# Optimization experiments

Hardware: AMD Instinct MI355X
Metric: run time of the kernel (lower is better)

The kernel has to match this reference:

```python
import jax, jax.numpy as jnp
import numpy as np

B, L, D, NH, V, T, CYC = 16, 512, 512, 8, 8000, 17, 2
HD = D // NH


def _attn(q, kv, qw, qb, kw, kb, vw, vb, ow, ob):
    # q: [N, Lq, D], kv: [N, Lk, D]; weights stored [in, out] (= torch W.T)
    N, Lq, _ = q.shape
    Lk = kv.shape[1]
    Q = (q @ qw + qb).reshape(N, Lq, NH, HD)
    K = (kv @ kw + kb).reshape(N, Lk, NH, HD)
    Vv = (kv @ vw + vb).reshape(N, Lk, NH, HD)
    scores = jnp.einsum('nqhd,nkhd->nhqk', Q, K) / np.float32(np.sqrt(HD))
    probs = jax.nn.softmax(scores, axis=-1)
    ctx = jnp.einsum('nhqk,nkhd->nqhd', probs, Vv).reshape(N, Lq, D)
    return ctx @ ow + ob


def _ln(x, w, b, eps=1e-12):
    u = x.mean(-1, keepdims=True)
    s = ((x - u) ** 2).mean(-1, keepdims=True)
    return w * (x - u) / jnp.sqrt(s + eps) + b


def setup_inputs() -> dict:
    key = jax.random.key(0)
    ks = jax.random.split(key, 32)
    p = {}
    p['tokens'] = jax.random.randint(ks[0], (B, L, 1), 0, V)
    p['masks'] = jnp.ones((B, L), dtype=jnp.int64)
    p['heads'] = jax.random.randint(ks[1], (B, L), 0, 2)
    p['tails'] = jax.random.randint(ks[2], (B, L), 0, 2)
    p['char_emb'] = jax.random.normal(ks[3], (V, D), jnp.float32) * 0.02
    i = 4
    for pre in ('sat', 'rel'):
        for nm in ('q', 'k', 'v', 'o'):
            p[f'{pre}_{nm}w'] = jax.random.normal(ks[i], (D, D), jnp.float32) * 0.02
            p[f'{pre}_{nm}b'] = jnp.zeros((D,), jnp.float32)
            i += 1
    p['ln_sat_w'] = jnp.ones((D,), jnp.float32)
    p['ln_sat_b'] = jnp.zeros((D,), jnp.float32)
    p['ln_rel_w'] = jnp.ones((D,), jnp.float32)
    p['ln_rel_b'] = jnp.zeros((D,), jnp.float32)
    p['ofc_w'] = jax.random.normal(ks[i], (D, T), jnp.float32) * 0.02
    p['ofc_b'] = jnp.zeros((T,), jnp.float32)
    return p


def reference(tokens, masks, heads, tails, char_emb,
              sat_qw, sat_qb, sat_kw, sat_kb, sat_vw, sat_vb, sat_ow, sat_ob,
              rel_qw, rel_qb, rel_kw, rel_kb, rel_vw, rel_vb, rel_ow, rel_ob,
              ln_sat_w, ln_sat_b, ln_rel_w, ln_rel_b, ofc_w, ofc_b):
    e = char_emb[tokens[:, :, 0]]  # [B, L, D]
    h = e
    s = e.mean(axis=1)  # relay token [B, D] (avg_pool2d over seq)
    for _ in range(CYC):
        # backward cycle_shift in the source is a correct roll-by-(-1)
        h_last = jnp.roll(h, -1, axis=1)
        # forward cycle_shift in the source is sequential in-place: result[:,0]=h[:,-1],
        # result[:,i>=1]=h[:,0] (the write at i=0 propagates). Reproduced faithfully.
        h_next = jnp.concatenate(
            [h[:, -1:, :], jnp.broadcast_to(h[:, :1, :], (B, L - 1, D))], axis=1)
        sm = jnp.broadcast_to(s[:, None, :], (B, L, D))
        c = jnp.stack([h_last, h, h_next, e, sm], axis=2).reshape(B * L, 5, D)
        hq = h.reshape(B * L, 1, D)
        a = _attn(hq, c, sat_qw, sat_qb, sat_kw, sat_kb, sat_vw, sat_vb, sat_ow, sat_ob)
        h = _ln(jax.nn.relu(a), ln_sat_w, ln_sat_b).reshape(B, L, D)
        mc = jnp.concatenate([s[:, None, :], h], axis=1)  # [B, L+1, D]
        r = _attn(s[:, None, :], mc, rel_qw, rel_qb, rel_kw, rel_kb, rel_vw, rel_vb, rel_ow, rel_ob)
        s = _ln(jax.nn.relu(r), ln_rel_w, ln_rel_b)[:, 0, :]
    logits = h @ ofc_w + ofc_b  # [B, L, T]
    return logits
```

## Files before the change

kernel.cpp:

```cpp
#include <hip/hip_runtime.h>
#include <hip/hip_bf16.h>

typedef __hip_bfloat16 bf16;

#define BB 16
#define LL 512
#define DD 512
#define NHH 8
#define HDD 64
#define TT 17
#define MM (BB*LL)
#define RCH 8
#define RCK 65

typedef __attribute__((ext_vector_type(8))) short bfrag;
typedef __attribute__((ext_vector_type(4))) float ffrag;
typedef __attribute__((ext_vector_type(8))) unsigned short us8;

static __device__ __forceinline__ void gld16(const void* g, void* l){
  __builtin_amdgcn_global_load_lds((const __attribute__((address_space(1))) void*)g,
                                   (__attribute__((address_space(3))) void*)l, 16, 0, 0);
}
static __device__ __forceinline__ float us2f(unsigned short u){
  unsigned int v = ((unsigned int)u) << 16;
  float f; __builtin_memcpy(&f, &v, 4); return f;
}
static __device__ __forceinline__ float hsum8(float v){
  v += __shfl_xor(v, 1);
  v += __shfl_xor(v, 2);
  v += __shfl_xor(v, 4);
  return v;
}

__global__ __launch_bounds__(256)
void emean(const int* __restrict__ tokens, const float* __restrict__ emb,
           bf16* __restrict__ ebf, float* __restrict__ mpart){
  int blk = blockIdx.x;
  int b = blk >> 4, lc = blk & 15;
  int t = threadIdx.x;
  __shared__ int toks[32];
  if (t < 32) toks[t] = tokens[b*LL + lc*32 + t];
  __syncthreads();
  bf16* eb = ebf + ((size_t)b*LL + lc*32)*DD;
  for (int d = t; d < DD; d += 256){
    float acc = 0.f;
    #pragma unroll 4
    for (int l = 0; l < 32; l++){
      float v = emb[(size_t)toks[l]*DD + d];
      eb[(size_t)l*DD + d] = __float2bfloat16(v);
      acc += v;
    }
    mpart[(size_t)blk*DD + d] = acc;
  }
}
__global__ void mean2(const float* __restrict__ part, float* __restrict__ s){
  int i = blockIdx.x*256 + threadIdx.x;
  int b = i >> 9, d = i & 511;
  float acc = 0.f;
  #pragma unroll
  for (int c = 0; c < 16; c++) acc += part[(size_t)(b*16 + c)*DD + d];
  s[i] = acc * (1.0f/LL);
}

__global__ void prep_w(const float* __restrict__ i0, const float* __restrict__ i1,
                       const float* __restrict__ i2, const float* __restrict__ i3,
                       const float* __restrict__ i4, const float* __restrict__ i5,
                       const float* __restrict__ wlog,
                       bf16* __restrict__ o0, bf16* __restrict__ o1,
                       bf16* __restrict__ o2, bf16* __restrict__ o3,
                       bf16* __restrict__ o4, bf16* __restrict__ o5,
                       bf16* __restrict__ olog){
  int z = blockIdx.z;
  int tx = threadIdx.x, ty = threadIdx.y;
  if (z == 6){
    int tid = ty*32 + tx;
    int i = ((blockIdx.y*16 + blockIdx.x) << 8) + tid;
    int row = i >> 9, k = i & 511;
    olog[i] = __float2bfloat16(row < TT ? wlog[(size_t)k*TT + row] : 0.f);
    return;
  }
  __shared__ float tile[32][33];
  const float* in = (z==0)?i0:(z==1)?i1:(z==2)?i2:(z==3)?i3:(z==4)?i4:i5;
  bf16* out       = (z==0)?o0:(z==1)?o1:(z==2)?o2:(z==3)?o3:(z==4)?o4:o5;
  int bx = blockIdx.x*32, by = blockIdx.y*32;
  #pragma unroll
  for (int j = 0; j < 32; j += 8)
    tile[ty + j][tx] = in[(size_t)(by + ty + j)*DD + bx + tx];
  __syncthreads();
  #pragma unroll
  for (int j = 0; j < 32; j += 8)
    out[(size_t)(bx + ty + j)*DD + by + tx] = __float2bfloat16(tile[tx][ty + j]);
}

__global__ __launch_bounds__(256)
void gemm_mfma_bf(const bf16* __restrict__ A, const bf16* __restrict__ Wt,
                  const float* __restrict__ b0, const float* __restrict__ b1,
                  const float* __restrict__ b2, const float* __restrict__ b3,
                  const float* __restrict__ b4,
                  bf16* __restrict__ D0, int ld0,
                  bf16* __restrict__ D1, int ld1, int split){
  const int K = 512;
  __shared__ bf16 As[128*32];
  __shared__ bf16 Bs[128*32];
  int t = threadIdx.x;
  int wave = t >> 6, lane = t & 63;
  int id = blockIdx.x;
  int bm = (((id & 7) << 3) | ((id >> 3) & 7)) * 128;
  int bn = (id >> 6) * 128;
  int wm = (wave & 1) * 64, wn = (wave >> 1) * 64;
  ffrag acc[4][4];
  #pragma unroll
  for (int i = 0; i < 4; i++)
    #pragma unroll
    for (int j = 0; j < 4; j++) acc[i][j] = (ffrag){0.f,0.f,0.f,0.f};

  int srow = t >> 2;
  int scol = (t & 3) * 8;
  const bf16* gA = A  + (size_t)(bm + srow)*K + scol;
  const bf16* gB = Wt + (size_t)(bn + srow)*K + scol;
  char* lA = (char*)As + 16*t;
  char* lB = (char*)Bs + 16*t;
  int q = lane >> 4, r = lane & 15;

  for (int k0 = 0; k0 < K; k0 += 32){
    gld16(gA + k0,          lA);
    gld16(gA + 64*K + k0,   lA + 4096);
    gld16(gB + k0,          lB);
    gld16(gB + 64*K + k0,   lB + 4096);
    __syncthreads();
    bfrag af[4], bfv[4];
    #pragma unroll
    for (int i = 0; i < 4; i++){
      af[i]  = *(const bfrag*)(As + (wm + i*16 + r)*32 + q*8);
      bfv[i] = *(const bfrag*)(Bs + (wn + i*16 + r)*32 + q*8);
    }
    #pragma unroll
    for (int i = 0; i < 4; i++)
      #pragma unroll
      for (int j = 0; j < 4; j++)
        acc[i][j] = __builtin_amdgcn_mfma_f32_16x16x32_bf16(af[i], bfv[j], acc[i][j], 0, 0, 0);
    __syncthreads();
  }
  #pragma unroll
  for (int i = 0; i < 4; i++){
    #pragma unroll
    for (int j = 0; j < 4; j++){
      int row = bm + wm + i*16 + q*4;
      int col = bn + wn + j*16 + r;
      const float* bp = (col < 512) ? b0 : (col < 1024) ? b1 :
                        (col < 1536) ? b2 : (col < 2048) ? b3 : b4;
      float bias = bp[col & 511];
      bf16* D; int ld;
      if (col < split){ D = D0 + (size_t)row*ld0 + col;         ld = ld0; }
      else            { D = D1 + (size_t)row*ld1 + (col-split); ld = ld1; }
      #pragma unroll
      for (int g = 0; g < 4; g++)
        D[(size_t)g*ld] = __float2bfloat16(acc[i][j][g] + bias);
    }
  }
}

__global__ __launch_bounds__(256)
void gemm_logits(const bf16* __restrict__ A, const bf16* __restrict__ Wt,
                 const float* __restrict__ bias, float* __restrict__ C){
  const int K = 512;
  __shared__ bf16 As[128*32];
  __shared__ bf16 Bs[128*32];
  int t = threadIdx.x;
  int wave = t >> 6, lane = t & 63;
  int bm = blockIdx.y * 128;
  int wm = (wave & 1) * 64, wn = (wave >> 1) * 64;
  ffrag acc[2];
  acc[0] = (ffrag){0.f,0.f,0.f,0.f};
  acc[1] = (ffrag){0.f,0.f,0.f,0.f};

  int srow = t >> 2;
  int scol = (t & 3) * 8;
  const bf16* gA = A  + (size_t)(bm + srow)*K + scol;
  const bf16* gB = Wt + (size_t)srow*K + scol;
  char* lA = (char*)As + 16*t;
  char* lB = (char*)Bs + 16*t;
  int q = lane >> 4, r = lane & 15;

  for (int k0 = 0; k0 < K; k0 += 32){
    gld16(gA + k0,          lA);
    gld16(gA + 64*K + k0,   lA + 4096);
    gld16(gB + k0,          lB);
    gld16(gB + 64*K + k0,   lB + 4096);
    __syncthreads();
    if (wn == 0){
      #pragma unroll
      for (int i = 0; i < 4; i++){
        bfrag af = *(const bfrag*)(As + (wm + i*16 + r)*32 + q*8);
        if (i < 2){
          bfrag bfv = *(const bfrag*)(Bs + (i*16 + r)*32 + q*8);
        }
      }
      bfrag bf0 = *(const bfrag*)(Bs + (0*16 + r)*32 + q*8);
      bfrag bf1 = *(const bfrag*)(Bs + (1*16 + r)*32 + q*8);
      #pragma unroll
      for (int i = 0; i < 4; i++){
        bfrag af = *(const bfrag*)(As + (wm + i*16 + r)*32 + q*8);
        (void)af; (void)bf0; (void)bf1;
      }
    }
    __syncthreads();
  }
  (void)acc; (void)bias; (void)C; (void)wn;
}

__global__ __launch_bounds__(256)
void gemm_logits2(const bf16* __restrict__ A, const bf16* __restrict__ Wt,
                  const float* __restrict__ bias, float* __restrict__ C){
  const int K = 512;
  __shared__ bf16 As[128*32];
  __shared__ bf16 Bs[128*32];
  int t = threadIdx.x;
  int wave = t >> 6, lane = t & 63;
  int bm = blockIdx.y * 128;
  int wm = (wave & 1) * 64, wn = (wave >> 1) * 64;
  ffrag acc[4][2];
  #pragma unroll
  for (int i = 0; i < 4; i++){ acc[i][0] = (ffrag){0,0,0,0}; acc[i][1] = (ffrag){0,0,0,0}; }

  int srow = t >> 2;
  int scol = (t & 3) * 8;
  const bf16* gA = A  + (size_t)(bm + srow)*K + scol;
  const bf16* gB = Wt + (size_t)srow*K + scol;
  char* lA = (char*)As + 16*t;
  char* lB = (char*)Bs + 16*t;
  int q = lane >> 4, r = lane & 15;

  for (int k0 = 0; k0 < K; k0 += 32){
    gld16(gA + k0,          lA);
    gld16(gA + 64*K + k0,   lA + 4096);
    gld16(gB + k0,          lB);
    gld16(gB + 64*K + k0,   lB + 4096);
    __syncthreads();
    if (wn == 0){
      bfrag bf0 = *(const bfrag*)(Bs + (r)*32 + q*8);
      bfrag bf1 = *(const bfrag*)(Bs + (16 + r)*32 + q*8);
      #pragma unroll
      for (int i = 0; i < 4; i++){
        bfrag af = *(const bfrag*)(As + (wm + i*16 + r)*32 + q*8);
        acc[i][0] = __builtin_amdgcn_mfma_f32_16x16x32_bf16(af, bf0, acc[i][0], 0, 0, 0);
        acc[i][1] = __builtin_amdgcn_mfma_f32_16x16x32_bf16(af, bf1, acc[i][1], 0, 0, 0);
      }
    }
    __syncthreads();
  }
  if (wn == 0){
    #pragma unroll
    for (int i = 0; i < 4; i++){
      #pragma unroll
      for (int j = 0; j < 2; j++){
        int row = bm + wm + i*16 + q*4;
        int col = j*16 + r;
        if (col < TT){
          float bias_v = bias[col];
          #pragma unroll
          for (int g = 0; g < 4; g++)
            C[(size_t)(row + g)*TT + col] = acc[i][j][g] + bias_v;
        }
      }
    }
  }
}

__global__ __launch_bounds__(256)
void s_proj(const float* __restrict__ A,
            const float* __restrict__ W0, const float* __restrict__ W1,
            const float* __restrict__ W2, const float* __restrict__ W3,
            const float* __restrict__ W4,
            const float* __restrict__ bias0, const float* __restrict__ bias1,
            const float* __restrict__ bias2, const float* __restrict__ bias3,
            const float* __restrict__ bias4,
            float* __restrict__ O0, float* __restrict__ O1,
            float* __restrict__ O2, float* __restrict__ O3,
            float* __restrict__ O4,
            int ldc0, int ldc1, int ldc2, int ldc3, int ldc4){
  __shared__ float part[8][32][17];
  int t = threadIdx.x;
  int n = t & 31, kg = t >> 5;
  int wi = blockIdx.x >> 4, ch = blockIdx.x & 15;
  const float* W  = (wi==0)?W0:(wi==1)?W1:(wi==2)?W2:(wi==3)?W3:W4;
  const float* bs = (wi==0)?bias0:(wi==1)?bias1:(wi==2)?bias2:(wi==3)?bias3:bias4;
  float* O  = (wi==0)?O0:(wi==1)?O1:(wi==2)?O2:(wi==3)?O3:O4;
  int ldc   = (wi==0)?ldc0:(wi==1)?ldc1:(wi==2)?ldc2:(wi==3)?ldc3:ldc4;
  int col = ch*32 + n;
  float acc[16];
  #pragma unroll
  for (int m = 0; m < 16; m++) acc[m] = 0.f;
  const float* Wp = W + (size_t)(kg*64)*512 + col;
  const float* Ap = A + kg*64;
  for (int k = 0; k < 64; k++){
    float w = Wp[(size_t)k*512];
    #pragma unroll
    for (int m = 0; m < 16; m++) acc[m] = fmaf(Ap[m*512 + k], w, acc[m]);
  }
  #pragma unroll
  for (int m = 0; m < 16; m++) part[kg][n][m] = acc[m];
  __syncthreads();
  for (int o = t; o < 512; o += 256){
    int m = o >> 5, nn = o & 31;
    float v = 0.f;
    #pragma unroll
    for (int g = 0; g < 8; g++) v += part[g][nn][m];
    O[(size_t)m*ldc + ch*32 + nn] = v + bs[ch*32 + nn];
  }
}

__global__ __launch_bounds__(256)
void sat_attn(const bf16* __restrict__ qp, int sq,
              const bf16* __restrict__ kp, const bf16* __restrict__ vp, int skv,
              const bf16* __restrict__ KeVe, const float* __restrict__ KsVs,
              bf16* __restrict__ ctx){
  int tok = blockIdx.x*4 + (threadIdx.x >> 6);
  int l = threadIdx.x & 63;
  int b = tok >> 9, li = tok & 511;
  int off = l*8;
  int t0 = (b << 9) | ((li + 1) & 511);
  int t2 = (b << 9) | (li == 0 ? 511 : 0);

  float qf[8];
  { us8 q8 = *(const us8*)(qp + (size_t)tok*sq + off);
    #pragma unroll
    for (int g = 0; g < 8; g++) qf[g] = us2f(q8[g]); }

  float sc[5];
  int rows[3] = {t0, tok, t2};
  #pragma unroll
  for (int j = 0; j < 3; j++){
    us8 k8 = *(const us8*)(kp + (size_t)rows[j]*skv + off);
    float a = 0.f;
    #pragma unroll
    for (int g = 0; g < 8; g++) a += qf[g]*us2f(k8[g]);
    sc[j] = hsum8(a) * 0.125f;
  }
  { us8 k8 = *(const us8*)(KeVe + (size_t)tok*1024 + off);
    float a = 0.f;
    #pragma unroll
    for (int g = 0; g < 8; g++) a += qf[g]*us2f(k8[g]);
    sc[3] = hsum8(a) * 0.125f; }
  { const float* ks = KsVs + (size_t)b*1024 + off;
    float4 f0 = *(const float4*)ks, f1 = *(const float4*)(ks + 4);
    float a = qf[0]*f0.x + qf[1]*f0.y + qf[2]*f0.z + qf[3]*f0.w
            + qf[4]*f1.x + qf[5]*f1.y + qf[6]*f1.z + qf[7]*f1.w;
    sc[4] = hsum8(a) * 0.125f; }

  float m = fmaxf(fmaxf(fmaxf(sc[0],sc[1]), fmaxf(sc[2],sc[3])), sc[4]);
  float p[5], den = 0.f;
  #pragma unroll
  for (int j = 0; j < 5; j++){ p[j] = __expf(sc[j]-m); den += p[j]; }
  float inv = 1.0f/den;

  float o[8];
  #pragma unroll
  for (int g = 0; g < 8; g++) o[g] = 0.f;
  #pragma unroll
  for (int j = 0; j < 3; j++){
    us8 v8 = *(const us8*)(vp + (size_t)rows[j]*skv + off);
    #pragma unroll
    for (int g = 0; g < 8; g++) o[g] += p[j]*us2f(v8[g]);
  }
  { us8 v8 = *(const us8*)(KeVe + (size_t)tok*1024 + 512 + off);
    #pragma unroll
    for (int g = 0; g < 8; g++) o[g] += p[3]*us2f(v8[g]); }
  { const float* vs = KsVs + (size_t)b*1024 + 512 + off;
    float4 f0 = *(const float4*)vs, f1 = *(const float4*)(vs + 4);
    o[0] += p[4]*f0.x; o[1] += p[4]*f0.y; o[2] += p[4]*f0.z; o[3] += p[4]*f0.w;
    o[4] += p[4]*f1.x; o[5] += p[4]*f1.y; o[6] += p[4]*f1.z; o[7] += p[4]*f1.w; }

  bf16 ob[8];
  #pragma unroll
  for (int g = 0; g < 8; g++) ob[g] = __float2bfloat16(o[g]*inv);
  *(us8*)(ctx + (size_t)tok*DD + off) = *(const us8*)ob;
}

__global__ __launch_bounds__(256)
void rel_part(const float* __restrict__ q, const float* __restrict__ Ksr,
              const float* __restrict__ Vsr, const bf16* __restrict__ KV,
              float* __restrict__ pws){
  int ch = blockIdx.x, hh = blockIdx.y, b = blockIdx.z;
  int t = threadIdx.x;
  int base = hh * HDD;
  __shared__ __align__(16) float qs[64];
  __shared__ float sc[RCK];
  __shared__ float red[256];
  __shared__ float part[4][64];
  int j0 = ch * RCK;
  int nk = min(513 - j0, RCK);
  if (t < 64) qs[t] = q[(size_t)b*DD + base + t];
  __syncthreads();
  if (t < nk){
    int j = j0 + t;
    float a = 0.f;
    if (j == 0){
      const float* kr = Ksr + (size_t)b*DD + base;
      #pragma unroll
      for (int d = 0; d < 64; d += 4){
        float4 k4 = *(const float4*)(kr + d);
        float4 q4 = *(const float4*)(qs + d);
        a += q4.x*k4.x + q4.y*k4.y + q4.z*k4.z + q4.w*k4.w;
      }
    } else {
      const bf16* kr = KV + ((size_t)b*LL + j - 1)*1024 + base;
      #pragma unroll
      for (int d = 0; d < 64; d += 8){
        us8 k8 = *(const us8*)(kr + d);
        #pragma unroll
        for (int g = 0; g < 8; g++) a += qs[d+g] * us2f(k8[g]);
      }
    }
    sc[t] = a * 0.125f;
  }
  __syncthreads();
  red[t] = (t < nk) ? sc[t] : -1e30f; __syncthreads();
  for (int st = 128; st; st >>= 1){ if (t < st) red[t] = fmaxf(red[t], red[t+st]); __syncthreads(); }
  float m = red[0]; __syncthreads();
  if (t < nk) sc[t] = __expf(sc[t] - m);
  __syncthreads();
  red[t] = (t < nk) ? sc[t] : 0.f; __syncthreads();
  for (int st = 128; st; st >>= 1){ if (t < st) red[t] += red[t+st]; __syncthreads(); }
  float l = red[0];
  int d = t & 63, c2 = t >> 6;
  float a = 0.f;
  for (int j = c2; j < nk; j += 4){
    int gj = j0 + j;
    float vv = (gj == 0) ? Vsr[(size_t)b*DD + base + d]
                         : __bfloat162float(KV[((size_t)b*LL + gj - 1)*1024 + 512 + base + d]);
    a += sc[j] * vv;
  }
  part[c2][d] = a; __syncthreads();
  float* o = pws + (((size_t)(b*NHH + hh))*RCH + ch) * 66;
  if (t < 64) o[t] = part[0][t] + part[1][t] + part[2][t] + part[3][t];
  else if (t == 64) o[64] = m;
  else if (t == 65) o[65] = l;
}

__global__ __launch_bounds__(256)
void rel_tail(const float* __restrict__ pws, const float* __restrict__ W,
              const float* __restrict__ bias, const float* __restrict__ lnw,
              const float* __restrict__ lnb, float* __restrict__ s){
  int b = blockIdx.x;
  int t = threadIdx.x;
  __shared__ float crs[512];
  __shared__ float red[256];
  for (int o = t; o < 512; o += 256){
    int hh = o >> 6, d = o & 63;
    const float* p = pws + ((size_t)(b*NHH + hh))*RCH*66;
    float M = -1e30f;
    #pragma unroll
    for (int c = 0; c < RCH; c++) M = fmaxf(M, p[c*66 + 64]);
    float den = 0.f, acc = 0.f;
    #pragma unroll
    for (int c = 0; c < RCH; c++){
      float w = __expf(p[c*66 + 64] - M);
      den += w * p[c*66 + 65];
      acc += w * p[c*66 + d];
    }
    crs[o] = acc / den;
  }
  __syncthreads();
  int n0 = t, n1 = t + 256;
  float a0 = 0.f, a1 = 0.f;
  for (int k = 0; k < 512; k++){
    float c = crs[k];
    a0 = fmaf(c, W[(size_t)k*512 + n0], a0);
    a1 = fmaf(c, W[(size_t)k*512 + n1], a1);
  }
  a0 += bias[n0]; a1 += bias[n1];
  float v0 = fmaxf(a0, 0.f), v1 = fmaxf(a1, 0.f);
  red[t] = v0 + v1; __syncthreads();
  for (int st = 128; st; st >>= 1){ if (t < st) red[t] += red[t+st]; __syncthreads(); }
  float u = red[0] * (1.0f/DD); __syncthreads();
  float d0 = v0 - u, d1 = v1 - u;
  red[t] = d0*d0 + d1*d1; __syncthreads();
  for (int st = 128; st; st >>= 1){ if (t < st) red[t] += red[t+st]; __syncthreads(); }
  float inv = rsqrtf(red[0] * (1.0f/DD) + 1e-12f);
  s[(size_t)b*DD + n0] = lnw[n0]*d0*inv + lnb[n0];
  s[(size_t)b*DD + n1] = lnw[n1]*d1*inv + lnb[n1];
}

__global__ void relu_ln_bf(const bf16* __restrict__ X, const float* __restrict__ w,
                           const float* __restrict__ bn, bf16* __restrict__ Ybf){
  int row = blockIdx.x;
  int tid = threadIdx.x;
  __shared__ float red[256];
  const bf16* x = X + (size_t)row*DD;
  float v0 = fmaxf(__bfloat162float(x[tid]), 0.f);
  float v1 = fmaxf(__bfloat162float(x[tid+256]), 0.f);
  red[tid] = v0 + v1;
  __syncthreads();
  for (int st = 128; st; st >>= 1){ if (tid < st) red[tid] += red[tid+st]; __syncthreads(); }
  float u = red[0] * (1.0f/DD);
  __syncthreads();
  float d0 = v0 - u, d1 = v1 - u;
  red[tid] = d0*d0 + d1*d1;
  __syncthreads();
  for (int st = 128; st; st >>= 1){ if (tid < st) red[tid] += red[tid+st]; __syncthreads(); }
  float var = red[0] * (1.0f/DD);
  float inv = rsqrtf(var + 1e-12f);
  Ybf[(size_t)row*DD + tid]       = __float2bfloat16(w[tid]    *d0*inv + bn[tid]);
  Ybf[(size_t)row*DD + tid + 256] = __float2bfloat16(w[tid+256]*d1*inv + bn[tid+256]);
}

extern "C" void kernel_launch(void* const* d_in, const int* in_sizes, int n_in,
                              void* d_out, int out_size, void* d_ws, size_t ws_size,
                              hipStream_t stream) {
  const int*   tokens  = (const int*)  d_in[0];
  const float* emb     = (const float*)d_in[4];
  const float* sat_qw  = (const float*)d_in[5];
  const float* sat_qb  = (const float*)d_in[6];
  const float* sat_kw  = (const float*)d_in[7];
  const float* sat_kb  = (const float*)d_in[8];
  const float* sat_vw  = (const float*)d_in[9];
  const float* sat_vb  = (const float*)d_in[10];
  const float* sat_ow  = (const float*)d_in[11];
  const float* sat_ob  = (const float*)d_in[12];
  const float* rel_qw  = (const float*)d_in[13];
  const float* rel_qb  = (const float*)d_in[14];
  const float* rel_kw  = (const float*)d_in[15];
  const float* rel_kb  = (const float*)d_in[16];
  const float* rel_vw  = (const float*)d_in[17];
  const float* rel_vb  = (const float*)d_in[18];
  const float* rel_ow  = (const float*)d_in[19];
  const float* rel_ob  = (const float*)d_in[20];
  const float* ln_sat_w= (const float*)d_in[21];
  const float* ln_sat_b= (const float*)d_in[22];
  const float* ln_rel_w= (const float*)d_in[23];
  const float* ln_rel_b= (const float*)d_in[24];
  const float* ofc_w   = (const float*)d_in[25];
  const float* ofc_b   = (const float*)d_in[26];

  char* p = (char*)d_ws;
  auto alloc = [&](size_t bytes) -> char* {
    char* r = p; p += (bytes + 255) & ~(size_t)255; return r;
  };
  const size_t BIGH = (size_t)MM*DD*2;
  bf16*  ebf   = (bf16*) alloc(BIGH);
  bf16*  qkv   = (bf16*) alloc(3*BIGH);
  bf16*  kvbuf = (bf16*) alloc(2*BIGH);
  bf16*  KeVe  = (bf16*) alloc(2*BIGH);
  bf16*  qbuf  = (bf16*) alloc(BIGH);
  bf16*  ctxbf = (bf16*) alloc(BIGH);
  bf16*  WtAll = (bf16*) alloc((size_t)2560*512*2);
  bf16*  WtO   = (bf16*) alloc((size_t)512*512*2);
  bf16*  WtLog = (bf16*) alloc((size_t)128*512*2);
  float* s     = (float*)alloc(BB*DD*4);
  float* KsVs  = (float*)alloc(BB*1024*4);
  float* qr    = (float*)alloc(BB*DD*4);
  float* Ksr   = (float*)alloc(BB*DD*4);
  float* Vsr   = (float*)alloc(BB*DD*4);
  float* mpart = (float*)alloc((size_t)256*DD*4);
  float* pws   = (float*)alloc((size_t)BB*NHH*RCH*66*4);
  bf16*  hbf   = ebf;
  bf16*  aout  = qkv;

  emean<<<256, 256, 0, stream>>>(tokens, emb, ebf, mpart);
  mean2<<<32, 256, 0, stream>>>(mpart, s);

  prep_w<<<dim3(16,16,7), dim3(32,8), 0, stream>>>(
      sat_qw, sat_kw, sat_vw, rel_kw, rel_vw, sat_ow, ofc_w,
      WtAll, WtAll + (size_t)512*512, WtAll + (size_t)1024*512,
      WtAll + (size_t)1536*512, WtAll + (size_t)2048*512, WtO, WtLog);

  gemm_mfma_bf<<<12*64, 256, 0, stream>>>(ebf, WtAll,
      sat_qb, sat_kb, sat_vb, sat_vb, sat_vb, qbuf, 512, KeVe, 1024, 512);
  s_proj<<<80, 256, 0, stream>>>(s,
      sat_kw, sat_vw, rel_qw, rel_kw, rel_vw,
      sat_kb, sat_vb, rel_qb, rel_kb, rel_vb,
      KsVs, KsVs + 512, qr, Ksr, Vsr,
      1024, 1024, 512, 512, 512);
  sat_attn<<<MM/4, 256, 0, stream>>>(qbuf, 512, KeVe, KeVe + 512, 1024,
                                     KeVe, KsVs, ctxbf);
  gemm_mfma_bf<<<4*64, 256, 0, stream>>>(ctxbf, WtO,
      sat_ob, sat_ob, sat_ob, sat_ob, sat_ob, aout, 512, aout, 512, 512);
  relu_ln_bf<<<MM, 256, 0, stream>>>(aout, ln_sat_w, ln_sat_b, hbf);
  gemm_mfma_bf<<<20*64, 256, 0, stream>>>(hbf, WtAll,
      sat_qb, sat_kb, sat_vb, rel_kb, rel_vb, qkv, 1536, kvbuf, 1024, 1536);
  rel_part<<<dim3(RCH, NHH, BB), 256, 0, stream>>>(qr, Ksr, Vsr, kvbuf, pws);
  rel_tail<<<BB, 256, 0, stream>>>(pws, rel_ow, rel_ob, ln_rel_w, ln_rel_b, s);

  s_proj<<<32, 256, 0, stream>>>(s,
      sat_kw, sat_vw, sat_vw, sat_vw, sat_vw,
      sat_kb, sat_vb, sat_vb, sat_vb, sat_vb,
      KsVs, KsVs + 512, Ksr, Ksr, Ksr,
      1024, 1024, 512, 512, 512);
  sat_attn<<<MM/4, 256, 0, stream>>>(qkv, 1536, qkv + 512, qkv + 1024, 1536,
                                     KeVe, KsVs, ctxbf);
  gemm_mfma_bf<<<4*64, 256, 0, stream>>>(ctxbf, WtO,
      sat_ob, sat_ob, sat_ob, sat_ob, sat_ob, aout, 512, aout, 512, 512);
  relu_ln_bf<<<MM, 256, 0, stream>>>(aout, ln_sat_w, ln_sat_b, hbf);

  gemm_logits2<<<dim3(1,64), 256, 0, stream>>>(hbf, WtLog, ofc_b, (float*)d_out);
}
```

Before: 336.3 us.

## Fuse whole forward into one cooperative persistent megakernel with grid syncs

Replaces the sequence of separate kernel launches with a single cooperative kernel that runs each stage as work units over a persistent grid, separated by grid-wide barriers. A per-launch fallback path is kept. It also swizzles the LDS column layout in the GEMM tiles to reduce bank conflicts. The s-projection is restructured so each batch row is handled by one block with a serial K loop. The aim is to remove launch gaps between stages, at the cost of grid-sync overhead, a grid capped at about two blocks per CU for large stages, and a slower single-block fp32 s-projection.

```diff
diff --git a/kernel.cpp b/kernel.cpp
--- a/kernel.cpp
+++ b/kernel.cpp
@@ -1,6 +1,8 @@
 #include <hip/hip_runtime.h>
 #include <hip/hip_bf16.h>
-
+#include <hip/hip_cooperative_groups.h>
+
+namespace cg = cooperative_groups;
 typedef __hip_bfloat16 bf16;
 
 #define BB 16
@@ -17,6 +19,16 @@
 typedef __attribute__((ext_vector_type(4))) float ffrag;
 typedef __attribute__((ext_vector_type(8))) unsigned short us8;
 
+struct Params {
+  const int* tokens;
+  const float* emb;
+  const float *sat_qw, *sat_qb, *sat_kw, *sat_kb, *sat_vw, *sat_vb, *sat_ow, *sat_ob;
+  const float *rel_qw, *rel_qb, *rel_kw, *rel_kb, *rel_vw, *rel_vb, *rel_ow, *rel_ob;
+  const float *ln_sat_w, *ln_sat_b, *ln_rel_w, *ln_rel_b, *ofc_w, *ofc_b;
+  bf16 *ebf, *qkv, *kvbuf, *KeVe, *qbuf, *ctxbf, *WtAll, *WtO, *WtLog;
+  float *KsVs, *qr, *Ksr, *Vsr, *mpart, *pws, *out;
+};
+
 static __device__ __forceinline__ void gld16(const void* g, void* l){
   __builtin_amdgcn_global_load_lds((const __attribute__((address_space(1))) void*)g,
                                    (__attribute__((address_space(3))) void*)l, 16, 0, 0);
@@ -26,63 +38,43 @@
   float f; __builtin_memcpy(&f, &v, 4); return f;
 }
 static __device__ __forceinline__ float hsum8(float v){
-  v += __shfl_xor(v, 1);
-  v += __shfl_xor(v, 2);
-  v += __shfl_xor(v, 4);
+  v += __shfl_xor(v, 1); v += __shfl_xor(v, 2); v += __shfl_xor(v, 4);
   return v;
 }
 
-__global__ __launch_bounds__(256)
-void emean(const int* __restrict__ tokens, const float* __restrict__ emb,
-           bf16* __restrict__ ebf, float* __restrict__ mpart){
-  int blk = blockIdx.x;
-  int b = blk >> 4, lc = blk & 15;
-  int t = threadIdx.x;
-  __shared__ int toks[32];
-  if (t < 32) toks[t] = tokens[b*LL + lc*32 + t];
-  __syncthreads();
-  bf16* eb = ebf + ((size_t)b*LL + lc*32)*DD;
+static __device__ void emean_unit(int u, int t, char* sm, const Params& P){
+  int* toks = (int*)sm;
+  int b = u >> 4, lc = u & 15;
+  if (t < 32) toks[t] = P.tokens[b*LL + lc*32 + t];
+  __syncthreads();
+  bf16* eb = P.ebf + ((size_t)b*LL + lc*32)*DD;
   for (int d = t; d < DD; d += 256){
     float acc = 0.f;
     #pragma unroll 4
     for (int l = 0; l < 32; l++){
-      float v = emb[(size_t)toks[l]*DD + d];
+      float v = P.emb[(size_t)toks[l]*DD + d];
       eb[(size_t)l*DD + d] = __float2bfloat16(v);
       acc += v;
     }
-    mpart[(size_t)blk*DD + d] = acc;
-  }
-}
-__global__ void mean2(const float* __restrict__ part, float* __restrict__ s){
-  int i = blockIdx.x*256 + threadIdx.x;
-  int b = i >> 9, d = i & 511;
-  float acc = 0.f;
-  #pragma unroll
-  for (int c = 0; c < 16; c++) acc += part[(size_t)(b*16 + c)*DD + d];
-  s[i] = acc * (1.0f/LL);
-}
-
-__global__ void prep_w(const float* __restrict__ i0, const float* __restrict__ i1,
-                       const float* __restrict__ i2, const float* __restrict__ i3,
-                       const float* __restrict__ i4, const float* __restrict__ i5,
-                       const float* __restrict__ wlog,
-                       bf16* __restrict__ o0, bf16* __restrict__ o1,
-                       bf16* __restrict__ o2, bf16* __restrict__ o3,
-                       bf16* __restrict__ o4, bf16* __restrict__ o5,
-                       bf16* __restrict__ olog){
-  int z = blockIdx.z;
-  int tx = threadIdx.x, ty = threadIdx.y;
+    P.mpart[(size_t)u*DD + d] = acc;
+  }
+  __syncthreads();
+}
+
+static __device__ void prep_unit(int u, int t, char* sm, const Params& P){
+  int z = u >> 8, xy = u & 255;
+  int tx = t & 31, ty = t >> 5;
   if (z == 6){
-    int tid = ty*32 + tx;
-    int i = ((blockIdx.y*16 + blockIdx.x) << 8) + tid;
+    int i = (xy << 8) + t;
     int row = i >> 9, k = i & 511;
-    olog[i] = __float2bfloat16(row < TT ? wlog[(size_t)k*TT + row] : 0.f);
+    P.WtLog[i] = __float2bfloat16(row < TT ? P.ofc_w[(size_t)k*TT + row] : 0.f);
     return;
   }
-  __shared__ float tile[32][33];
-  const float* in = (z==0)?i0:(z==1)?i1:(z==2)?i2:(z==3)?i3:(z==4)?i4:i5;
-  bf16* out       = (z==0)?o0:(z==1)?o1:(z==2)?o2:(z==3)?o3:(z==4)?o4:o5;
-  int bx = blockIdx.x*32, by = blockIdx.y*32;
+  float (*tile)[33] = (float(*)[33])sm;
+  const float* in = (z==0)?P.sat_qw:(z==1)?P.sat_kw:(z==2)?P.sat_vw:
+                    (z==3)?P.rel_kw:(z==4)?P.rel_vw:P.sat_ow;
+  bf16* out = (z<5) ? (P.WtAll + (size_t)z*512*512) : P.WtO;
+  int bx = (xy & 15)*32, by = (xy >> 4)*32;
   #pragma unroll
   for (int j = 0; j < 32; j += 8)
     tile[ty + j][tx] = in[(size_t)(by + ty + j)*DD + bx + tx];
@@ -90,21 +82,44 @@
   #pragma unroll
   for (int j = 0; j < 32; j += 8)
     out[(size_t)(bx + ty + j)*DD + by + tx] = __float2bfloat16(tile[tx][ty + j]);
-}
-
-__global__ __launch_bounds__(256)
-void gemm_mfma_bf(const bf16* __restrict__ A, const bf16* __restrict__ Wt,
-                  const float* __restrict__ b0, const float* __restrict__ b1,
-                  const float* __restrict__ b2, const float* __restrict__ b3,
-                  const float* __restrict__ b4,
-                  bf16* __restrict__ D0, int ld0,
-                  bf16* __restrict__ D1, int ld1, int split){
+  __syncthreads();
+}
+
+static __device__ void sfull_unit(int b, int t, char* sm, const Params& P){
+  float* sL = (float*)sm;
+  for (int d = t; d < 512; d += 256){
+    float a = 0.f;
+    #pragma unroll
+    for (int c = 0; c < 16; c++) a += P.mpart[(size_t)(b*16 + c)*DD + d];
+    sL[d] = a * (1.0f/LL);
+  }
+  __syncthreads();
+  const float* Ws[5] = {P.sat_kw, P.sat_vw, P.rel_qw, P.rel_kw, P.rel_vw};
+  const float* Bb[5] = {P.sat_kb, P.sat_vb, P.rel_qb, P.rel_kb, P.rel_vb};
+  float* Os[5] = {P.KsVs + (size_t)b*1024, P.KsVs + (size_t)b*1024 + 512,
+                  P.qr + (size_t)b*512, P.Ksr + (size_t)b*512, P.Vsr + (size_t)b*512};
+  #pragma unroll
+  for (int w = 0; w < 5; w++){
+    const float* W = Ws[w];
+    float a0 = Bb[w][t], a1 = Bb[w][t+256];
+    for (int k = 0; k < 512; k++){
+      float sv = sL[k];
+      a0 = fmaf(sv, W[(size_t)k*512 + t],       a0);
+      a1 = fmaf(sv, W[(size_t)k*512 + t + 256], a1);
+    }
+    Os[w][t] = a0; Os[w][t+256] = a1;
+  }
+  __syncthreads();
+}
+
+static __device__ void gemm_unit(int id, int t, char* sm,
+    const bf16* __restrict__ A, const bf16* __restrict__ Wt,
+    const float* b0, const float* b1, const float* b2, const float* b3, const float* b4,
+    bf16* D0, int ld0, bf16* D1, int ld1, int split){
   const int K = 512;
-  __shared__ bf16 As[128*32];
-  __shared__ bf16 Bs[128*32];
-  int t = threadIdx.x;
+  bf16* As = (bf16*)sm;
+  bf16* Bs = (bf16*)(sm + 8192);
   int wave = t >> 6, lane = t & 63;
-  int id = blockIdx.x;
   int bm = (((id & 7) << 3) | ((id >> 3) & 7)) * 128;
   int bn = (id >> 6) * 128;
   int wm = (wave & 1) * 64, wn = (wave >> 1) * 64;
@@ -115,12 +130,13 @@
     for (int j = 0; j < 4; j++) acc[i][j] = (ffrag){0.f,0.f,0.f,0.f};
 
   int srow = t >> 2;
-  int scol = (t & 3) * 8;
+  int scol = ((((t & 3) - ((t >> 3) & 3)) & 3)) * 8;
   const bf16* gA = A  + (size_t)(bm + srow)*K + scol;
   const bf16* gB = Wt + (size_t)(bn + srow)*K + scol;
   char* lA = (char*)As + 16*t;
   char* lB = (char*)Bs + 16*t;
   int q = lane >> 4, r = lane & 15;
+  int cs = (((q + (r >> 1)) & 3)) * 8;
 
   for (int k0 = 0; k0 < K; k0 += 32){
     gld16(gA + k0,          lA);
@@ -131,8 +147,8 @@
     bfrag af[4], bfv[4];
     #pragma unroll
     for (int i = 0; i < 4; i++){
-      af[i]  = *(const bfrag*)(As + (wm + i*16 + r)*32 + q*8);
-      bfv[i] = *(const bfrag*)(Bs + (wn + i*16 + r)*32 + q*8);
+      af[i]  = *(const bfrag*)(As + (wm + i*16 + r)*32 + cs);
+      bfv[i] = *(const bfrag*)(Bs + (wn + i*16 + r)*32 + cs);
     }
     #pragma unroll
     for (int i = 0; i < 4; i++)
@@ -160,27 +176,24 @@
   }
 }
 
-__global__ __launch_bounds__(256)
-void gemm_logits(const bf16* __restrict__ A, const bf16* __restrict__ Wt,
-                 const float* __restrict__ bias, float* __restrict__ C){
+static __device__ void logits_unit(int u, int t, char* sm, const Params& P){
   const int K = 512;
-  __shared__ bf16 As[128*32];
-  __shared__ bf16 Bs[128*32];
-  int t = threadIdx.x;
+  bf16* As = (bf16*)sm;
+  bf16* Bs = (bf16*)(sm + 8192);
   int wave = t >> 6, lane = t & 63;
-  int bm = blockIdx.y * 128;
+  int bm = u * 128;
   int wm = (wave & 1) * 64, wn = (wave >> 1) * 64;
-  ffrag acc[2];
-  acc[0] = (ffrag){0.f,0.f,0.f,0.f};
-  acc[1] = (ffrag){0.f,0.f,0.f,0.f};
-
+  ffrag acc[4][2];
+  #pragma unroll
+  for (int i = 0; i < 4; i++){ acc[i][0] = (ffrag){0,0,0,0}; acc[i][1] = (ffrag){0,0,0,0}; }
   int srow = t >> 2;
-  int scol = (t & 3) * 8;
-  const bf16* gA = A  + (size_t)(bm + srow)*K + scol;
-  const bf16* gB = Wt + (size_t)srow*K + scol;
+  int scol = ((((t & 3) - ((t >> 3) & 3)) & 3)) * 8;
+  const bf16* gA = P.ebf + (size_t)(bm + srow)*K + scol;
+  const bf16* gB = P.WtLog + (size_t)srow*K + scol;
   char* lA = (char*)As + 16*t;
   char* lB = (char*)Bs + 16*t;
   int q = lane >> 4, r = lane & 15;
+  int cs = (((q + (r >> 1)) & 3)) * 8;
 
   for (int k0 = 0; k0 < K; k0 += 32){
     gld16(gA + k0,          lA);
@@ -189,60 +202,11 @@
     gld16(gB + 64*K + k0,   lB + 4096);
     __syncthreads();
     if (wn == 0){
+      bfrag bf0 = *(const bfrag*)(Bs + (r)*32 + cs);
+      bfrag bf1 = *(const bfrag*)(Bs + (16 + r)*32 + cs);
       #pragma unroll
       for (int i = 0; i < 4; i++){
-        bfrag af = *(const bfrag*)(As + (wm + i*16 + r)*32 + q*8);
-        if (i < 2){
-          bfrag bfv = *(const bfrag*)(Bs + (i*16 + r)*32 + q*8);
-        }
-      }
-      bfrag bf0 = *(const bfrag*)(Bs + (0*16 + r)*32 + q*8);
-      bfrag bf1 = *(const bfrag*)(Bs + (1*16 + r)*32 + q*8);
-      #pragma unroll
-      for (int i = 0; i < 4; i++){
-        bfrag af = *(const bfrag*)(As + (wm + i*16 + r)*32 + q*8);
-        (void)af; (void)bf0; (void)bf1;
-      }
-    }
-    __syncthreads();
-  }
-  (void)acc; (void)bias; (void)C; (void)wn;
-}
-
-__global__ __launch_bounds__(256)
-void gemm_logits2(const bf16* __restrict__ A, const bf16* __restrict__ Wt,
-                  const float* __restrict__ bias, float* __restrict__ C){
-  const int K = 512;
-  __shared__ bf16 As[128*32];
-  __shared__ bf16 Bs[128*32];
-  int t = threadIdx.x;
-  int wave = t >> 6, lane = t & 63;
-  int bm = blockIdx.y * 128;
-  int wm = (wave & 1) * 64, wn = (wave >> 1) * 64;
-  ffrag acc[4][2];
-  #pragma unroll
-  for (int i = 0; i < 4; i++){ acc[i][0] = (ffrag){0,0,0,0}; acc[i][1] = (ffrag){0,0,0,0}; }
-
-  int srow = t >> 2;
-  int scol = (t & 3) * 8;
-  const bf16* gA = A  + (size_t)(bm + srow)*K + scol;
-  const bf16* gB = Wt + (size_t)srow*K + scol;
-  char* lA = (char*)As + 16*t;
-  char* lB = (char*)Bs + 16*t;
-  int q = lane >> 4, r = lane & 15;
-
-  for (int k0 = 0; k0 < K; k0 += 32){
-    gld16(gA + k0,          lA);
-    gld16(gA + 64*K + k0,   lA + 4096);
-    gld16(gB + k0,          lB);
-    gld16(gB + 64*K + k0,   lB + 4096);
-    __syncthreads();
-    if (wn == 0){
-      bfrag bf0 = *(const bfrag*)(Bs + (r)*32 + q*8);
-      bfrag bf1 = *(const bfrag*)(Bs + (16 + r)*32 + q*8);
-      #pragma unroll
-      for (int i = 0; i < 4; i++){
-        bfrag af = *(const bfrag*)(As + (wm + i*16 + r)*32 + q*8);
+        bfrag af = *(const bfrag*)(As + (wm + i*16 + r)*32 + cs);
         acc[i][0] = __builtin_amdgcn_mfma_f32_16x16x32_bf16(af, bf0, acc[i][0], 0, 0, 0);
         acc[i][1] = __builtin_amdgcn_mfma_f32_16x16x32_bf16(af, bf1, acc[i][1], 0, 0, 0);
       }
@@ -251,82 +215,33 @@
   }
   if (wn == 0){
     #pragma unroll
-    for (int i = 0; i < 4; i++){
+    for (int i = 0; i < 4; i++)
       #pragma unroll
       for (int j = 0; j < 2; j++){
         int row = bm + wm + i*16 + q*4;
         int col = j*16 + r;
         if (col < TT){
-          float bias_v = bias[col];
+          float bv = P.ofc_b[col];
           #pragma unroll
           for (int g = 0; g < 4; g++)
-            C[(size_t)(row + g)*TT + col] = acc[i][j][g] + bias_v;
+            P.out[(size_t)(row + g)*TT + col] = acc[i][j][g] + bv;
         }
       }
-    }
-  }
-}
-
-__global__ __launch_bounds__(256)
-void s_proj(const float* __restrict__ A,
-            const float* __restrict__ W0, const float* __restrict__ W1,
-            const float* __restrict__ W2, const float* __restrict__ W3,
-            const float* __restrict__ W4,
-            const float* __restrict__ bias0, const float* __restrict__ bias1,
-            const float* __restrict__ bias2, const float* __restrict__ bias3,
-            const float* __restrict__ bias4,
-            float* __restrict__ O0, float* __restrict__ O1,
-            float* __restrict__ O2, float* __restrict__ O3,
-            float* __restrict__ O4,
-            int ldc0, int ldc1, int ldc2, int ldc3, int ldc4){
-  __shared__ float part[8][32][17];
-  int t = threadIdx.x;
-  int n = t & 31, kg = t >> 5;
-  int wi = blockIdx.x >> 4, ch = blockIdx.x & 15;
-  const float* W  = (wi==0)?W0:(wi==1)?W1:(wi==2)?W2:(wi==3)?W3:W4;
-  const float* bs = (wi==0)?bias0:(wi==1)?bias1:(wi==2)?bias2:(wi==3)?bias3:bias4;
-  float* O  = (wi==0)?O0:(wi==1)?O1:(wi==2)?O2:(wi==3)?O3:O4;
-  int ldc   = (wi==0)?ldc0:(wi==1)?ldc1:(wi==2)?ldc2:(wi==3)?ldc3:ldc4;
-  int col = ch*32 + n;
-  float acc[16];
-  #pragma unroll
-  for (int m = 0; m < 16; m++) acc[m] = 0.f;
-  const float* Wp = W + (size_t)(kg*64)*512 + col;
-  const float* Ap = A + kg*64;
-  for (int k = 0; k < 64; k++){
-    float w = Wp[(size_t)k*512];
-    #pragma unroll
-    for (int m = 0; m < 16; m++) acc[m] = fmaf(Ap[m*512 + k], w, acc[m]);
-  }
-  #pragma unroll
-  for (int m = 0; m < 16; m++) part[kg][n][m] = acc[m];
-  __syncthreads();
-  for (int o = t; o < 512; o += 256){
-    int m = o >> 5, nn = o & 31;
-    float v = 0.f;
-    #pragma unroll
-    for (int g = 0; g < 8; g++) v += part[g][nn][m];
-    O[(size_t)m*ldc + ch*32 + nn] = v + bs[ch*32 + nn];
-  }
-}
-
-__global__ __launch_bounds__(256)
-void sat_attn(const bf16* __restrict__ qp, int sq,
-              const bf16* __restrict__ kp, const bf16* __restrict__ vp, int skv,
-              const bf16* __restrict__ KeVe, const float* __restrict__ KsVs,
-              bf16* __restrict__ ctx){
-  int tok = blockIdx.x*4 + (threadIdx.x >> 6);
-  int l = threadIdx.x & 63;
+  }
+}
+
+static __device__ void sat_unit(int u, int t, const Params& P,
+    const bf16* qp, int sq, const bf16* kp, const bf16* vp, int skv){
+  int tok = u*4 + (t >> 6);
+  int l = t & 63;
   int b = tok >> 9, li = tok & 511;
   int off = l*8;
   int t0 = (b << 9) | ((li + 1) & 511);
   int t2 = (b << 9) | (li == 0 ? 511 : 0);
-
   float qf[8];
   { us8 q8 = *(const us8*)(qp + (size_t)tok*sq + off);
     #pragma unroll
     for (int g = 0; g < 8; g++) qf[g] = us2f(q8[g]); }
-
   float sc[5];
   int rows[3] = {t0, tok, t2};
   #pragma unroll
@@ -337,23 +252,21 @@
     for (int g = 0; g < 8; g++) a += qf[g]*us2f(k8[g]);
     sc[j] = hsum8(a) * 0.125f;
   }
-  { us8 k8 = *(const us8*)(KeVe + (size_t)tok*1024 + off);
+  { us8 k8 = *(const us8*)(P.KeVe + (size_t)tok*1024 + off);
     float a = 0.f;
     #pragma unroll
     for (int g = 0; g < 8; g++) a += qf[g]*us2f(k8[g]);
     sc[3] = hsum8(a) * 0.125f; }
-  { const float* ks = KsVs + (size_t)b*1024 + off;
+  { const float* ks = P.KsVs + (size_t)b*1024 + off;
     float4 f0 = *(const float4*)ks, f1 = *(const float4*)(ks + 4);
     float a = qf[0]*f0.x + qf[1]*f0.y + qf[2]*f0.z + qf[3]*f0.w
             + qf[4]*f1.x + qf[5]*f1.y + qf[6]*f1.z + qf[7]*f1.w;
     sc[4] = hsum8(a) * 0.125f; }
-
   float m = fmaxf(fmaxf(fmaxf(sc[0],sc[1]), fmaxf(sc[2],sc[3])), sc[4]);
-  float p[5], den = 0.f;
-  #pragma unroll
-  for (int j = 0; j < 5; j++){ p[j] = __expf(sc[j]-m); den += p[j]; }
+  float pr[5], den = 0.f;
+  #pragma unroll
+  for (int j = 0; j < 5; j++){ pr[j] = __expf(sc[j]-m); den += pr[j]; }
   float inv = 1.0f/den;
-
   float o[8];
   #pragma unroll
   for (int g = 0; g < 8; g++) o[g] = 0.f;
@@ -361,42 +274,55 @@
   for (int j = 0; j < 3; j++){
     us8 v8 = *(const us8*)(vp + (size_t)rows[j]*skv + off);
     #pragma unroll
-    for (int g = 0; g < 8; g++) o[g] += p[j]*us2f(v8[g]);
-  }
-  { us8 v8 = *(const us8*)(KeVe + (size_t)tok*1024 + 512 + off);
-    #pragma unroll
-    for (int g = 0; g < 8; g++) o[g] += p[3]*us2f(v8[g]); }
-  { const float* vs = KsVs + (size_t)b*1024 + 512 + off;
+    for (int g = 0; g < 8; g++) o[g] += pr[j]*us2f(v8[g]);
+  }
+  { us8 v8 = *(const us8*)(P.KeVe + (size_t)tok*1024 + 512 + off);
+    #pragma unroll
+    for (int g = 0; g < 8; g++) o[g] += pr[3]*us2f(v8[g]); }
+  { const float* vs = P.KsVs + (size_t)b*1024 + 512 + off;
     float4 f0 = *(const float4*)vs, f1 = *(const float4*)(vs + 4);
-    o[0] += p[4]*f0.x; o[1] += p[4]*f0.y; o[2] += p[4]*f0.z; o[3] += p[4]*f0.w;
-    o[4] += p[4]*f1.x; o[5] += p[4]*f1.y; o[6] += p[4]*f1.z; o[7] += p[4]*f1.w; }
-
+    o[0] += pr[4]*f0.x; o[1] += pr[4]*f0.y; o[2] += pr[4]*f0.z; o[3] += pr[4]*f0.w;
+    o[4] += pr[4]*f1.x; o[5] += pr[4]*f1.y; o[6] += pr[4]*f1.z; o[7] += pr[4]*f1.w; }
   bf16 ob[8];
   #pragma unroll
   for (int g = 0; g < 8; g++) ob[g] = __float2bfloat16(o[g]*inv);
-  *(us8*)(ctx + (size_t)tok*DD + off) = *(const us8*)ob;
-}
-
-__global__ __launch_bounds__(256)
-void rel_part(const float* __restrict__ q, const float* __restrict__ Ksr,
-              const float* __restrict__ Vsr, const bf16* __restrict__ KV,
-              float* __restrict__ pws){
-  int ch = blockIdx.x, hh = blockIdx.y, b = blockIdx.z;
-  int t = threadIdx.x;
+  *(us8*)(P.ctxbf + (size_t)tok*DD + off) = *(const us8*)ob;
+}
+
+static __device__ void ln_unit(int row, int t, char* sm, const Params& P,
+                               const bf16* X, bf16* Y){
+  float* red = (float*)sm;
+  const bf16* x = X + (size_t)row*DD;
+  float v0 = fmaxf(__bfloat162float(x[t]), 0.f);
+  float v1 = fmaxf(__bfloat162float(x[t+256]), 0.f);
+  red[t] = v0 + v1; __syncthreads();
+  for (int st = 128; st; st >>= 1){ if (t < st) red[t] += red[t+st]; __syncthreads(); }
+  float u = red[0] * (1.0f/DD); __syncthreads();
+  float d0 = v0 - u, d1 = v1 - u;
+  red[t] = d0*d0 + d1*d1; __syncthreads();
+  for (int st = 128; st; st >>= 1){ if (t < st) red[t] += red[t+st]; __syncthreads(); }
+  float inv = rsqrtf(red[0] * (1.0f/DD) + 1e-12f);
+  __syncthreads();
+  Y[(size_t)row*DD + t]       = __float2bfloat16(P.ln_sat_w[t]    *d0*inv + P.ln_sat_b[t]);
+  Y[(size_t)row*DD + t + 256] = __float2bfloat16(P.ln_sat_w[t+256]*d1*inv + P.ln_sat_b[t+256]);
+}
+
+static __device__ void relp_unit(int u, int t, char* sm, const Params& P){
+  int ch = u & 7, hh = (u >> 3) & 7, b = u >> 6;
+  float* qs   = (float*)sm;
+  float* sc   = (float*)(sm + 256);
+  float* red  = (float*)(sm + 1024);
+  float (*part)[64] = (float(*)[64])(sm + 2048);
   int base = hh * HDD;
-  __shared__ __align__(16) float qs[64];
-  __shared__ float sc[RCK];
-  __shared__ float red[256];
-  __shared__ float part[4][64];
   int j0 = ch * RCK;
   int nk = min(513 - j0, RCK);
-  if (t < 64) qs[t] = q[(size_t)b*DD + base + t];
+  if (t < 64) qs[t] = P.qr[(size_t)b*DD + base + t];
   __syncthreads();
   if (t < nk){
     int j = j0 + t;
     float a = 0.f;
     if (j == 0){
-      const float* kr = Ksr + (size_t)b*DD + base;
+      const float* kr = P.Ksr + (size_t)b*DD + base;
       #pragma unroll
       for (int d = 0; d < 64; d += 4){
         float4 k4 = *(const float4*)(kr + d);
@@ -404,7 +330,7 @@
         a += q4.x*k4.x + q4.y*k4.y + q4.z*k4.z + q4.w*k4.w;
       }
     } else {
-      const bf16* kr = KV + ((size_t)b*LL + j - 1)*1024 + base;
+      const bf16* kr = P.kvbuf + ((size_t)b*LL + j - 1)*1024 + base;
       #pragma unroll
       for (int d = 0; d < 64; d += 8){
         us8 k8 = *(const us8*)(kr + d);
@@ -427,28 +353,25 @@
   float a = 0.f;
   for (int j = c2; j < nk; j += 4){
     int gj = j0 + j;
-    float vv = (gj == 0) ? Vsr[(size_t)b*DD + base + d]
-                         : __bfloat162float(KV[((size_t)b*LL + gj - 1)*1024 + 512 + base + d]);
+    float vv = (gj == 0) ? P.Vsr[(size_t)b*DD + base + d]
+                         : __bfloat162float(P.kvbuf[((size_t)b*LL + gj - 1)*1024 + 512 + base + d]);
     a += sc[j] * vv;
   }
   part[c2][d] = a; __syncthreads();
-  float* o = pws + (((size_t)(b*NHH + hh))*RCH + ch) * 66;
+  float* o = P.pws + (((size_t)(b*NHH + hh))*RCH + ch) * 66;
   if (t < 64) o[t] = part[0][t] + part[1][t] + part[2][t] + part[3][t];
   else if (t == 64) o[64] = m;
   else if (t == 65) o[65] = l;
-}
-
-__global__ __launch_bounds__(256)
-void rel_tail(const float* __restrict__ pws, const float* __restrict__ W,
-              const float* __restrict__ bias, const float* __restrict__ lnw,
-              const float* __restrict__ lnb, float* __restrict__ s){
-  int b = blockIdx.x;
-  int t = threadIdx.x;
-  __shared__ float crs[512];
-  __shared__ float red[256];
+  __syncthreads();
+}
+
+static __device__ void reltail_unit(int b, int t, char* sm, const Params& P){
+  float* crs = (float*)sm;
+  float* red = (float*)(sm + 2048);
+  float* sL  = (float*)(sm + 3072);
   for (int o = t; o < 512; o += 256){
     int hh = o >> 6, d = o & 63;
-    const float* p = pws + ((size_t)(b*NHH + hh))*RCH*66;
+    const float* p = P.pws + ((size_t)(b*NHH + hh))*RCH*66;
     float M = -1e30f;
     #pragma unroll
     for (int c = 0; c < RCH; c++) M = fmaxf(M, p[c*66 + 64]);
@@ -463,13 +386,12 @@
   }
   __syncthreads();
   int n0 = t, n1 = t + 256;
-  float a0 = 0.f, a1 = 0.f;
+  float a0 = P.rel_ob[n0], a1 = P.rel_ob[n1];
   for (int k = 0; k < 512; k++){
     float c = crs[k];
-    a0 = fmaf(c, W[(size_t)k*512 + n0], a0);
-    a1 = fmaf(c, W[(size_t)k*512 + n1], a1);
-  }
-  a0 += bias[n0]; a1 += bias[n1];
+    a0 = fmaf(c, P.rel_ow[(size_t)k*512 + n0], a0);
+    a1 = fmaf(c, P.rel_ow[(size_t)k*512 + n1], a1);
+  }
   float v0 = fmaxf(a0, 0.f), v1 = fmaxf(a1, 0.f);
   red[t] = v0 + v1; __syncthreads();
   for (int st = 128; st; st >>= 1){ if (t < st) red[t] += red[t+st]; __syncthreads(); }
@@ -478,120 +400,193 @@
   red[t] = d0*d0 + d1*d1; __syncthreads();
   for (int st = 128; st; st >>= 1){ if (t < st) red[t] += red[t+st]; __syncthreads(); }
   float inv = rsqrtf(red[0] * (1.0f/DD) + 1e-12f);
-  s[(size_t)b*DD + n0] = lnw[n0]*d0*inv + lnb[n0];
-  s[(size_t)b*DD + n1] = lnw[n1]*d1*inv + lnb[n1];
-}
-
-__global__ void relu_ln_bf(const bf16* __restrict__ X, const float* __restrict__ w,
-                           const float* __restrict__ bn, bf16* __restrict__ Ybf){
-  int row = blockIdx.x;
-  int tid = threadIdx.x;
-  __shared__ float red[256];
-  const bf16* x = X + (size_t)row*DD;
-  float v0 = fmaxf(__bfloat162float(x[tid]), 0.f);
-  float v1 = fmaxf(__bfloat162float(x[tid+256]), 0.f);
-  red[tid] = v0 + v1;
-  __syncthreads();
-  for (int st = 128; st; st >>= 1){ if (tid < st) red[tid] += red[tid+st]; __syncthreads(); }
-  float u = red[0] * (1.0f/DD);
-  __syncthreads();
-  float d0 = v0 - u, d1 = v1 - u;
-  red[tid] = d0*d0 + d1*d1;
-  __syncthreads();
-  for (int st = 128; st; st >>= 1){ if (tid < st) red[tid] += red[tid+st]; __syncthreads(); }
-  float var = red[0] * (1.0f/DD);
-  float inv = rsqrtf(var + 1e-12f);
-  Ybf[(size_t)row*DD + tid]       = __float2bfloat16(w[tid]    *d0*inv + bn[tid]);
-  Ybf[(size_t)row*DD + tid + 256] = __float2bfloat16(w[tid+256]*d1*inv + bn[tid+256]);
+  sL[n0] = P.ln_rel_w[n0]*d0*inv + P.ln_rel_b[n0];
+  sL[n1] = P.ln_rel_w[n1]*d1*inv + P.ln_rel_b[n1];
+  __syncthreads();
+  const float* Ws[2] = {P.sat_kw, P.sat_vw};
+  const float* Bb[2] = {P.sat_kb, P.sat_vb};
+  #pragma unroll
+  for (int w = 0; w < 2; w++){
+    float b0 = Bb[w][n0], b1 = Bb[w][n1];
+    for (int k = 0; k < 512; k++){
+      float sv = sL[k];
+      b0 = fmaf(sv, Ws[w][(size_t)k*512 + n0], b0);
+      b1 = fmaf(sv, Ws[w][(size_t)k*512 + n1], b1);
+    }
+    P.KsVs[(size_t)b*1024 + w*512 + n0] = b0;
+    P.KsVs[(size_t)b*1024 + w*512 + n1] = b1;
+  }
+  __syncthreads();
+}
+
+__global__ __launch_bounds__(256, 2)
+void mega(Params P){
+  cg::grid_group g = cg::this_grid();
+  int bid = blockIdx.x, t = threadIdx.x;
+  int G = gridDim.x;
+  __shared__ __align__(16) char sm[16384];
+  bf16* hbf = P.ebf;
+  bf16* aout = P.qkv;
+
+  for (int u = bid; u < 256; u += G)  emean_unit(u, t, sm, P);
+  for (int u = bid; u < 1792; u += G) prep_unit(u, t, sm, P);
+  g.sync();
+
+  if (bid < 16) sfull_unit(bid, t, sm, P);
+  else for (int u = bid - 16; u < 12*64; u += G - 16)
+    gemm_unit(u, t, sm, P.ebf, P.WtAll, P.sat_qb, P.sat_kb, P.sat_vb, P.sat_vb, P.sat_vb,
+              P.qbuf, 512, P.KeVe, 1024, 512);
+  g.sync();
+
+  for (int u = bid; u < MM/4; u += G)
+    sat_unit(u, t, P, P.qbuf, 512, P.KeVe, P.KeVe + 512, 1024);
+  g.sync();
+
+  for (int u = bid; u < 4*64; u += G)
+    gemm_unit(u, t, sm, P.ctxbf, P.WtO, P.sat_ob, P.sat_ob, P.sat_ob, P.sat_ob, P.sat_ob,
+              aout, 512, aout, 512, 512);
+  g.sync();
+
+  for (int u = bid; u < MM; u += G) ln_unit(u, t, sm, P, aout, hbf);
+  g.sync();
+
+  for (int u = bid; u < 20*64; u += G)
+    gemm_unit(u, t, sm, hbf, P.WtAll, P.sat_qb, P.sat_kb, P.sat_vb, P.rel_kb, P.rel_vb,
+              P.qkv, 1536, P.kvbuf, 1024, 1536);
+  g.sync();
+
+  for (int u = bid; u < BB*NHH*RCH; u += G) relp_unit(u, t, sm, P);
+  g.sync();
+
+  for (int u = bid; u < BB; u += G) reltail_unit(u, t, sm, P);
+  g.sync();
+
+  for (int u = bid; u < MM/4; u += G)
+    sat_unit(u, t, P, P.qkv, 1536, P.qkv + 512, P.qkv + 1024, 1536);
+  g.sync();
+
+  for (int u = bid; u < 4*64; u += G)
+    gemm_unit(u, t, sm, P.ctxbf, P.WtO, P.sat_ob, P.sat_ob, P.sat_ob, P.sat_ob, P.sat_ob,
+              aout, 512, aout, 512, 512);
+  g.sync();
+
+  for (int u = bid; u < MM; u += G) ln_unit(u, t, sm, P, aout, hbf);
+  g.sync();
+
+  for (int u = bid; u < 64; u += G) logits_unit(u, t, sm, P);
+}
+
+__global__ __launch_bounds__(256) void k_emean(Params P){
+  __shared__ __align__(16) char sm[16384];
+  emean_unit(blockIdx.x, threadIdx.x, sm, P);
+}
+__global__ __launch_bounds__(256) void k_prep(Params P){
+  __shared__ __align__(16) char sm[16384];
+  prep_unit(blockIdx.x, threadIdx.x, sm, P);
+}
+__global__ __launch_bounds__(256) void k_sfull(Params P){
+  __shared__ __align__(16) char sm[16384];
+  sfull_unit(blockIdx.x, threadIdx.x, sm, P);
+}
+__global__ __launch_bounds__(256) void k_gemm(Params P, const bf16* A, const bf16* Wt,
+    const float* b0, const float* b1, const float* b2, const float* b3, const float* b4,
+    bf16* D0, int ld0, bf16* D1, int ld1, int split){
+  __shared__ __align__(16) char sm[16384];
+  gemm_unit(blockIdx.x, threadIdx.x, sm, A, Wt, b0, b1, b2, b3, b4, D0, ld0, D1, ld1, split);
+}
+__global__ __launch_bounds__(256) void k_sat(Params P, const bf16* qp, int sq,
+    const bf16* kp, const bf16* vp, int skv){
+  sat_unit(blockIdx.x, threadIdx.x, P, qp, sq, kp, vp, skv);
+}
+__global__ __launch_bounds__(256) void k_ln(Params P, const bf16* X, bf16* Y){
+  __shared__ __align__(16) char sm[16384];
+  ln_unit(blockIdx.x, threadIdx.x, sm, P, X, Y);
+}
+__global__ __launch_bounds__(256) void k_relp(Params P){
+  __shared__ __align__(16) char sm[16384];
+  relp_unit(blockIdx.x, threadIdx.x, sm, P);
+}
+__global__ __launch_bounds__(256) void k_reltail(Params P){
+  __shared__ __align__(16) char sm[16384];
+  reltail_unit(blockIdx.x, threadIdx.x, sm, P);
+}
+__global__ __launch_bounds__(256) void k_logits(Params P){
+  __shared__ __align__(16) char sm[16384];
+  logits_unit(blockIdx.x, threadIdx.x, sm, P);
 }
 
 extern "C" void kernel_launch(void* const* d_in, const int* in_sizes, int n_in,
                               void* d_out, int out_size, void* d_ws, size_t ws_size,
                               hipStream_t stream) {
-  const int*   tokens  = (const int*)  d_in[0];
-  const float* emb     = (const float*)d_in[4];
-  const float* sat_qw  = (const float*)d_in[5];
-  const float* sat_qb  = (const float*)d_in[6];
-  const float* sat_kw  = (const float*)d_in[7];
-  const float* sat_kb  = (const float*)d_in[8];
-  const float* sat_vw  = (const float*)d_in[9];
-  const float* sat_vb  = (const float*)d_in[10];
-  const float* sat_ow  = (const float*)d_in[11];
-  const float* sat_ob  = (const float*)d_in[12];
-  const float* rel_qw  = (const float*)d_in[13];
-  const float* rel_qb  = (const float*)d_in[14];
-  const float* rel_kw  = (const float*)d_in[15];
-  const float* rel_kb  = (const float*)d_in[16];
-  const float* rel_vw  = (const float*)d_in[17];
-  const float* rel_vb  = (const float*)d_in[18];
-  const float* rel_ow  = (const float*)d_in[19];
-  const float* rel_ob  = (const float*)d_in[20];
-  const float* ln_sat_w= (const float*)d_in[21];
-  const float* ln_sat_b= (const float*)d_in[22];
-  const float* ln_rel_w= (const float*)d_in[23];
-  const float* ln_rel_b= (const float*)d_in[24];
-  const float* ofc_w   = (const float*)d_in[25];
-  const float* ofc_b   = (const float*)d_in[26];
+  Params P;
+  P.tokens  = (const int*)  d_in[0];
+  P.emb     = (const float*)d_in[4];
+  P.sat_qw  = (const float*)d_in[5];  P.sat_qb = (const float*)d_in[6];
+  P.sat_kw  = (const float*)d_in[7];  P.sat_kb = (const float*)d_in[8];
+  P.sat_vw  = (const float*)d_in[9];  P.sat_vb = (const float*)d_in[10];
+  P.sat_ow  = (const float*)d_in[11]; P.sat_ob = (const float*)d_in[12];
+  P.rel_qw  = (const float*)d_in[13]; P.rel_qb = (const float*)d_in[14];
+  P.rel_kw  = (const float*)d_in[15]; P.rel_kb = (const float*)d_in[16];
+  P.rel_vw  = (const float*)d_in[17]; P.rel_vb = (const float*)d_in[18];
+  P.rel_ow  = (const float*)d_in[19]; P.rel_ob = (const float*)d_in[20];
+  P.ln_sat_w= (const float*)d_in[21]; P.ln_sat_b= (const float*)d_in[22];
+  P.ln_rel_w= (const float*)d_in[23]; P.ln_rel_b= (const float*)d_in[24];
+  P.ofc_w   = (const float*)d_in[25]; P.ofc_b  = (const float*)d_in[26];
 
   char* p = (char*)d_ws;
   auto alloc = [&](size_t bytes) -> char* {
     char* r = p; p += (bytes + 255) & ~(size_t)255; return r;
   };
   const size_t BIGH = (size_t)MM*DD*2;
-  bf16*  ebf   = (bf16*) alloc(BIGH);
-  bf16*  qkv   = (bf16*) alloc(3*BIGH);
-  bf16*  kvbuf = (bf16*) alloc(2*BIGH);
-  bf16*  KeVe  = (bf16*) alloc(2*BIGH);
-  bf16*  qbuf  = (bf16*) alloc(BIGH);
-  bf16*  ctxbf = (bf16*) alloc(BIGH);
-  bf16*  WtAll = (bf16*) alloc((size_t)2560*512*2);
-  bf16*  WtO   = (bf16*) alloc((size_t)512*512*2);
-  bf16*  WtLog = (bf16*) alloc((size_t)128*512*2);
-  float* s     = (float*)alloc(BB*DD*4);
-  float* KsVs  = (float*)alloc(BB*1024*4);
-  float* qr    = (float*)alloc(BB*DD*4);
-  float* Ksr   = (float*)alloc(BB*DD*4);
-  float* Vsr   = (float*)alloc(BB*DD*4);
-  float* mpart = (float*)alloc((size_t)256*DD*4);
-  float* pws   = (float*)alloc((size_t)BB*NHH*RCH*66*4);
-  bf16*  hbf   = ebf;
-  bf16*  aout  = qkv;
-
-  emean<<<256, 256, 0, stream>>>(tokens, emb, ebf, mpart);
-  mean2<<<32, 256, 0, stream>>>(mpart, s);
-
-  prep_w<<<dim3(16,16,7), dim3(32,8), 0, stream>>>(
-      sat_qw, sat_kw, sat_vw, rel_kw, rel_vw, sat_ow, ofc_w,
-      WtAll, WtAll + (size_t)512*512, WtAll + (size_t)1024*512,
-      WtAll + (size_t)1536*512, WtAll + (size_t)2048*512, WtO, WtLog);
-
-  gemm_mfma_bf<<<12*64, 256, 0, stream>>>(ebf, WtAll,
-      sat_qb, sat_kb, sat_vb, sat_vb, sat_vb, qbuf, 512, KeVe, 1024, 512);
-  s_proj<<<80, 256, 0, stream>>>(s,
-      sat_kw, sat_vw, rel_qw, rel_kw, rel_vw,
-      sat_kb, sat_vb, rel_qb, rel_kb, rel_vb,
-      KsVs, KsVs + 512, qr, Ksr, Vsr,
-      1024, 1024, 512, 512, 512);
-  sat_attn<<<MM/4, 256, 0, stream>>>(qbuf, 512, KeVe, KeVe + 512, 1024,
-                                     KeVe, KsVs, ctxbf);
-  gemm_mfma_bf<<<4*64, 256, 0, stream>>>(ctxbf, WtO,
-      sat_ob, sat_ob, sat_ob, sat_ob, sat_ob, aout, 512, aout, 512, 512);
-  relu_ln_bf<<<MM, 256, 0, stream>>>(aout, ln_sat_w, ln_sat_b, hbf);
-  gemm_mfma_bf<<<20*64, 256, 0, stream>>>(hbf, WtAll,
-      sat_qb, sat_kb, sat_vb, rel_kb, rel_vb, qkv, 1536, kvbuf, 1024, 1536);
-  rel_part<<<dim3(RCH, NHH, BB), 256, 0, stream>>>(qr, Ksr, Vsr, kvbuf, pws);
-  rel_tail<<<BB, 256, 0, stream>>>(pws, rel_ow, rel_ob, ln_rel_w, ln_rel_b, s);
-
-  s_proj<<<32, 256, 0, stream>>>(s,
-      sat_kw, sat_vw, sat_vw, sat_vw, sat_vw,
-      sat_kb, sat_vb, sat_vb, sat_vb, sat_vb,
-      KsVs, KsVs + 512, Ksr, Ksr, Ksr,
-      1024, 1024, 512, 512, 512);
-  sat_attn<<<MM/4, 256, 0, stream>>>(qkv, 1536, qkv + 512, qkv + 1024, 1536,
-                                     KeVe, KsVs, ctxbf);
-  gemm_mfma_bf<<<4*64, 256, 0, stream>>>(ctxbf, WtO,
-      sat_ob, sat_ob, sat_ob, sat_ob, sat_ob, aout, 512, aout, 512, 512);
-  relu_ln_bf<<<MM, 256, 0, stream>>>(aout, ln_sat_w, ln_sat_b, hbf);
-
-  gemm_logits2<<<dim3(1,64), 256, 0, stream>>>(hbf, WtLog, ofc_b, (float*)d_out);
-}
+  P.ebf   = (bf16*) alloc(BIGH);
+  P.qkv   = (bf16*) alloc(3*BIGH);
+  P.kvbuf = (bf16*) alloc(2*BIGH);
+  P.KeVe  = (bf16*) alloc(2*BIGH);
+  P.qbuf  = (bf16*) alloc(BIGH);
+  P.ctxbf = (bf16*) alloc(BIGH);
+  P.WtAll = (bf16*) alloc((size_t)2560*512*2);
+  P.WtO   = (bf16*) alloc((size_t)512*512*2);
+  P.WtLog = (bf16*) alloc((size_t)128*512*2);
+  P.KsVs  = (float*)alloc(BB*1024*4);
+  P.qr    = (float*)alloc(BB*DD*4);
+  P.Ksr   = (float*)alloc(BB*DD*4);
+  P.Vsr   = (float*)alloc(BB*DD*4);
+  P.mpart = (float*)alloc((size_t)256*DD*4);
+  P.pws   = (float*)alloc((size_t)BB*NHH*RCH*66*4);
+  P.out   = (float*)d_out;
+
+  int dev = 0; (void)hipGetDevice(&dev);
+  int coop = 0;
+  (void)hipDeviceGetAttribute(&coop, hipDeviceAttributeCooperativeLaunch, dev);
+  int maxB = 0;
+  (void)hipOccupancyMaxActiveBlocksPerMultiprocessor(&maxB, (const void*)mega, 256, 0);
+
+  bool done = false;
+  if (coop && maxB >= 1){
+    int grid = (maxB >= 2 ? 2 : 1) * 256;
+    void* args[] = { &P };
+    hipError_t e = hipLaunchCooperativeKernel((const void*)mega, dim3(grid), dim3(256),
+                                              args, 0, stream);
+    done = (e == hipSuccess);
+  }
+  if (!done){
+    k_emean<<<256, 256, 0, stream>>>(P);
+    k_prep<<<1792, 256, 0, stream>>>(P);
+    k_sfull<<<16, 256, 0, stream>>>(P);
+    k_gemm<<<768, 256, 0, stream>>>(P, P.ebf, P.WtAll,
+        P.sat_qb, P.sat_kb, P.sat_vb, P.sat_vb, P.sat_vb, P.qbuf, 512, P.KeVe, 1024, 512);
+    k_sat<<<MM/4, 256, 0, stream>>>(P, P.qbuf, 512, P.KeVe, P.KeVe + 512, 1024);
+    k_gemm<<<256, 256, 0, stream>>>(P, P.ctxbf, P.WtO,
+        P.sat_ob, P.sat_ob, P.sat_ob, P.sat_ob, P.sat_ob, P.qkv, 512, P.qkv, 512, 512);
+    k_ln<<<MM, 256, 0, stream>>>(P, P.qkv, P.ebf);
+    k_gemm<<<1280, 256, 0, stream>>>(P, P.ebf, P.WtAll,
+        P.sat_qb, P.sat_kb, P.sat_vb, P.rel_kb, P.rel_vb, P.qkv, 1536, P.kvbuf, 1024, 1536);
+    k_relp<<<BB*NHH*RCH, 256, 0, stream>>>(P);
+    k_reltail<<<BB, 256, 0, stream>>>(P);
+    k_sat<<<MM/4, 256, 0, stream>>>(P, P.qkv, 1536, P.qkv + 512, P.qkv + 1024, 1536);
+    k_gemm<<<256, 256, 0, stream>>>(P, P.ctxbf, P.WtO,
+        P.sat_ob, P.sat_ob, P.sat_ob, P.sat_ob, P.sat_ob, P.qkv, 512, P.qkv, 512, 512);
+    k_ln<<<MM, 256, 0, stream>>>(P, P.qkv, P.ebf);
+    k_logits<<<64, 256, 0, stream>>>(P);
+  }
+}
```

New measurement: 475.7 us. 41.4% more time.
